# Kernel tuning notes

Hardware: AMD Instinct MI355X
Metric: run time of the kernel (lower is better)

The kernel has to match this reference:

```python
import jax, jax.numpy as jnp
import numpy as np
import math

D_MODEL = 1024
N_HEADS = 16
RANK = 16
SCALE = 16.0
T_LEN = 2048
BSZ = 2


def setup_inputs() -> dict:
    key = jax.random.key(0)
    ks = jax.random.split(key, 12)
    d, r = D_MODEL, RANK
    inp = {
        "query": jax.random.normal(ks[0], (T_LEN, BSZ, d), dtype=jnp.float32),
        "key": jax.random.normal(ks[1], (T_LEN, BSZ, d), dtype=jnp.float32),
        "value": jax.random.normal(ks[2], (T_LEN, BSZ, d), dtype=jnp.float32),
        "need_weights": 0,
        "attn_mask": 0,
        "in_proj_weight": jax.random.normal(ks[3], (3 * d, d), dtype=jnp.float32) * 0.02,
        "in_proj_bias": jax.random.normal(ks[4], (3 * d,), dtype=jnp.float32) * 0.02,
        "out_w": jax.random.normal(ks[5], (d, d), dtype=jnp.float32) * 0.02,
        "out_b": jax.random.normal(ks[6], (d,), dtype=jnp.float32) * 0.02,
        "k_a": jax.random.normal(ks[7], (r, d), dtype=jnp.float32) * 0.02,
        "k_b": jax.random.normal(ks[8], (r, d), dtype=jnp.float32) * 0.02,
        "v_a": jax.random.normal(ks[9], (r, d), dtype=jnp.float32) * 0.02,
        "v_b": jax.random.normal(ks[10], (r, d), dtype=jnp.float32) * 0.02,
    }
    return inp


def reference(query, key, value, need_weights, attn_mask,
              in_proj_weight, in_proj_bias, out_w, out_b,
              k_a, k_b, v_a, v_b):
    # NOTE: original module computes q,k,v all from `query` (self-attention);
    # `key`, `value`, `need_weights`, `attn_mask` are unused in the math.
    T, B, d = query.shape
    H = N_HEADS
    hd = d // H
    qkv = query @ in_proj_weight.T + in_proj_bias  # (T, B, 3d)
    q, k, v = jnp.split(qkv, 3, axis=-1)
    s = SCALE / RANK
    # LoRA low-rank updates on K and V (computed from query)
    k = k + s * ((query @ k_a.T) @ k_b)
    v = v + s * ((query @ v_a.T) @ v_b)
    # split heads: (T, B, H, hd)
    qh = q.reshape(T, B, H, hd)
    kh = k.reshape(T, B, H, hd)
    vh = v.reshape(T, B, H, hd)
    scale = 1.0 / math.sqrt(hd)
    scores = jnp.einsum('tbhd,sbhd->bhts', qh * scale, kh)  # (B, H, T, T)
    attn = jax.nn.softmax(scores, axis=-1)
    out = jnp.einsum('bhts,sbhd->tbhd', attn, vh).reshape(T, B, d)
    out = out @ out_w.T + out_b
    return out
```

## Files before the change

kernel.cpp:

```cpp
#include <hip/hip_runtime.h>
#include <stdint.h>

#define DEVI __device__ __forceinline__

typedef unsigned short u16;
typedef __attribute__((ext_vector_type(4))) float f32x4;
typedef __attribute__((ext_vector_type(16))) float f32x16;
typedef __attribute__((ext_vector_type(8))) short bf16x8;
typedef __attribute__((ext_vector_type(2))) unsigned int u32x2;

constexpr int T_LEN = 2048;
constexpr int BSZ   = 2;
constexpr int DM    = 1024;
constexpr int NH    = 16;
constexpr int HD    = 64;
constexpr int MROWS = T_LEN * BSZ;
constexpr float LORA_S = 16.0f / 16.0f;
constexpr float QSCALE = 0.125f * 1.4426950408889634f;

DEVI u16 f2bf(float x) {
  union { float f; uint32_t u; } v; v.f = x;
  uint32_t r = (v.u + 0x7FFFu + ((v.u >> 16) & 1u)) >> 16;
  return (u16)r;
}

DEVI uint32_t pk2bf(float a, float b) {
  return (uint32_t)f2bf(a) | ((uint32_t)f2bf(b) << 16);
}

DEVI uint32_t e2r(float x) {
  union { float f; uint32_t u; } v;
  v.f = __builtin_amdgcn_exp2f(x);
  return v.u + 0x8000u;
}

DEVI void gload_lds16(const void* g, void* l) {
  __builtin_amdgcn_global_load_lds(
      (const __attribute__((address_space(1))) void*)g,
      (__attribute__((address_space(3))) void*)l, 16, 0, 0);
}

DEVI f32x4 mfma16(bf16x8 a, bf16x8 b, f32x4 c) {
  return __builtin_amdgcn_mfma_f32_16x16x32_bf16(a, b, c, 0, 0, 0);
}
DEVI f32x16 mfma32(bf16x8 a, bf16x8 b, f32x16 c) {
  return __builtin_amdgcn_mfma_f32_32x32x16_bf16(a, b, c, 0, 0, 0);
}

DEVI int kvswz(int rc, int l) { return rc * 128 + ((l ^ (rc & 15)) << 3); }

#define WAITBAR(N)                                        \
  do {                                                    \
    asm volatile("s_waitcnt vmcnt(" #N ")" ::: "memory"); \
    __builtin_amdgcn_sched_barrier(0);                    \
    __builtin_amdgcn_s_barrier();                         \
    __builtin_amdgcn_sched_barrier(0);                    \
  } while (0)

__global__ void prep_kernel(const float* __restrict__ query,
                            const float* __restrict__ W,
                            const float* __restrict__ ka, const float* __restrict__ kb,
                            const float* __restrict__ va, const float* __restrict__ vb,
                            const float* __restrict__ ow,
                            u16* __restrict__ Wm, u16* __restrict__ Wo,
                            u16* __restrict__ Aq) {
  const int W3 = 3 * DM * DM;
  const int WO = DM * DM;
  const int AQ = MROWS * DM;
  const int total = W3 + WO + AQ;
  for (int idx = blockIdx.x * blockDim.x + threadIdx.x; idx < total;
       idx += gridDim.x * blockDim.x) {
    if (idx < W3) {
      const int n = idx >> 10, k = idx & 1023;
      float w = W[idx];
      if (n >= 2 * DM) {
        const int n2 = n - 2 * DM;
        float a = 0.f;
#pragma unroll
        for (int r = 0; r < 16; ++r) a += va[r * DM + k] * vb[r * DM + n2];
        w += LORA_S * a;
      } else if (n >= DM) {
        const int n2 = n - DM;
        float a = 0.f;
#pragma unroll
        for (int r = 0; r < 16; ++r) a += ka[r * DM + k] * kb[r * DM + n2];
        w += LORA_S * a;
      }
      Wm[idx] = f2bf(w);
    } else if (idx < W3 + WO) {
      const int i = idx - W3;
      Wo[i] = f2bf(ow[i]);
    } else {
      const int i = idx - W3 - WO;
      Aq[i] = f2bf(query[i]);
    }
  }
}

template <int EPIL>
__global__ __launch_bounds__(256) void gemm_bt(
    const u16* __restrict__ A, const u16* __restrict__ Bt,
    const float* __restrict__ bias, float* __restrict__ Cf,
    u16* __restrict__ Qb, u16* __restrict__ Kb, u16* __restrict__ Vt,
    int M, int N, int K) {
  constexpr int BM = 128, BN = 128, BK = 32;
  __shared__ alignas(16) u16 SM[4][2][4096];
  const int tid = threadIdx.x;
  const int wv = tid >> 6, ln = tid & 63;
  const int l16 = ln & 15, lhi = ln >> 4;
  const int row0 = blockIdx.x * BM, col0 = blockIdx.y * BN;
  const int wr = (wv >> 1) * 64, wc = (wv & 1) * 64;

  f32x4 acc[4][4];
#pragma unroll
  for (int i = 0; i < 4; ++i)
#pragma unroll
    for (int j = 0; j < 4; ++j) acc[i][j] = f32x4{0.f, 0.f, 0.f, 0.f};

  const int lrA = wv * 16 + (ln >> 3);
  const int lrB = lrA + 8;
  const int s_ = ln & 7;
  const int la = s_ ^ (lrA & 7), lb = s_ ^ (lrB & 7);
  const int ra = lrA + 64 * (la >> 2), ca = (la & 3) * 8;
  const int rb = lrB + 64 * (lb >> 2), cb = (lb & 3) * 8;

  const u16* pa0 = A + (size_t)(row0 + ra) * K + ca;
  const u16* pa1 = A + (size_t)(row0 + rb) * K + cb;
  const u16* pb0 = Bt + (size_t)(col0 + ra) * K + ca;
  const u16* pb1 = Bt + (size_t)(col0 + rb) * K + cb;

  auto stagep = [&](int buf) {
    gload_lds16(pa0, &SM[buf][0][(wv * 16) * 64]);
    gload_lds16(pa1, &SM[buf][0][(wv * 16 + 8) * 64]);
    gload_lds16(pb0, &SM[buf][1][(wv * 16) * 64]);
    gload_lds16(pb1, &SM[buf][1][(wv * 16 + 8) * 64]);
    pa0 += BK; pa1 += BK; pb0 += BK; pb1 += BK;
  };

  auto compute = [&](int buf) {
    const u16* Al = SM[buf][0];
    const u16* Bl = SM[buf][1];
    bf16x8 af[4], bfr[4];
#pragma unroll
    for (int m = 0; m < 4; ++m) {
      const int r = wr + m * 16 + l16, lr = r & 63;
      const int sl = (lhi | ((r >> 6) << 2)) ^ (lr & 7);
      af[m] = *(const bf16x8*)&Al[lr * 64 + sl * 8];
    }
#pragma unroll
    for (int n = 0; n < 4; ++n) {
      const int r = wc + n * 16 + l16, lr = r & 63;
      const int sl = (lhi | ((r >> 6) << 2)) ^ (lr & 7);
      bfr[n] = *(const bf16x8*)&Bl[lr * 64 + sl * 8];
    }
#pragma unroll
    for (int m = 0; m < 4; ++m)
#pragma unroll
      for (int n = 0; n < 4; ++n) acc[m][n] = mfma16(af[m], bfr[n], acc[m][n]);
  };

  const int NS = K / BK;
  stagep(0); stagep(1); stagep(2);

  for (int t4 = 0; t4 < NS - 4; t4 += 4) {
    WAITBAR(8); compute(0); stagep(3);
    WAITBAR(8); compute(1); stagep(0);
    WAITBAR(8); compute(2); stagep(1);
    WAITBAR(8); compute(3); stagep(2);
  }
  WAITBAR(8); compute(0); stagep(3);
  WAITBAR(8); compute(1);
  WAITBAR(4); compute(2);
  WAITBAR(0); compute(3);

  if constexpr (EPIL == 0) {
    if (col0 >= 2 * DM) {
      u16* Cl = (u16*)SM;
      __syncthreads();
#pragma unroll
      for (int m = 0; m < 4; ++m)
#pragma unroll
        for (int n = 0; n < 4; ++n) {
          const int lc = wc + n * 16 + l16;
          const float bc = bias[col0 + lc];
#pragma unroll
          for (int r = 0; r < 4; ++r) {
            const int rl = wr + m * 16 + lhi * 4 + r;
            const int tl = rl >> 1, bb = rl & 1;
            Cl[lc * 128 + bb * 64 + (((tl >> 3) ^ (lc & 7)) << 3) + (tl & 7)] =
                f2bf(acc[m][n][r] + bc);
          }
        }
      __syncthreads();
      const int h0 = (col0 - 2 * DM) >> 6;
      const int t0 = row0 >> 1;
#pragma unroll
      for (int i = 0; i < 8; ++i) {
        const int cid = i * 256 + tid;
        const int lc = cid >> 4, bb = (cid >> 3) & 1, tc = cid & 7;
        bf16x8 ch = *(const bf16x8*)&Cl[lc * 128 + bb * 64 + ((tc ^ (lc & 7)) << 3)];
        const int h = h0 + (lc >> 6), dd = lc & 63;
        *(bf16x8*)&Vt[(((size_t)(bb * NH + h)) * HD + dd) * T_LEN + t0 + tc * 8] = ch;
      }
      return;
    }
  }

#pragma unroll
  for (int m = 0; m < 4; ++m) {
#pragma unroll
    for (int n = 0; n < 4; ++n) {
      const int col = col0 + wc + n * 16 + l16;
      const float bc = bias[col];
#pragma unroll
      for (int r = 0; r < 4; ++r) {
        const int row = row0 + wr + m * 16 + lhi * 4 + r;
        const float v = acc[m][n][r] + bc;
        if constexpr (EPIL == 0) {
          const int t = row >> 1, b = row & 1;
          if (col < DM) {
            const int h = col >> 6, dd = col & 63;
            Qb[(((size_t)(b * NH + h)) * T_LEN + t) * HD + dd] = f2bf(v * QSCALE);
          } else {
            const int c2 = col - DM, h = c2 >> 6, dd = c2 & 63;
            Kb[(((size_t)(b * NH + h)) * T_LEN + t) * HD + dd] = f2bf(v);
          }
        } else {
          Cf[(size_t)row * N + col] = v;
        }
      }
    }
  }
}

__global__ __launch_bounds__(256) void attn_kernel(const u16* __restrict__ Qb,
                                                   const u16* __restrict__ Kb,
                                                   const u16* __restrict__ Vt,
                                                   u16* __restrict__ Ob) {
  constexpr int KBLK = 64;
  constexpr int NT = T_LEN / KBLK;
  __shared__ alignas(16) u16 KV[4][2][32 * 128];

  const int tid = threadIdx.x;
  const int wv = tid >> 6, ln = tid & 63;
  const int l32 = ln & 31, hi = ln >> 5;

  const int bid = blockIdx.x;
  const int lb = (bid & 7) * 64 + (bid >> 3);
  const int bh = lb >> 4;
  const int b = bh >> 4, h = bh & 15;
  const int q0 = (lb & 15) * 128 + wv * 32;

  const u16* Qh = Qb + (size_t)bh * T_LEN * HD;
  const u16* Kh = Kb + (size_t)bh * T_LEN * HD;
  const u16* Vh = Vt + (size_t)bh * HD * T_LEN;

  bf16x8 qf[4];
#pragma unroll
  for (int kd = 0; kd < 4; ++kd)
    qf[kd] = *(const bf16x8*)&Qh[(size_t)(q0 + l32) * HD + kd * 16 + hi * 8];

  bf16x8 ones;
#pragma unroll
  for (int i = 0; i < 8; ++i) ones[i] = (short)0x3F80;

  f32x16 ot[2] = {f32x16{}, f32x16{}};
  f32x16 lacc = f32x16{};

  const int g_row = ln >> 4;
  const int g_s   = ln & 15;
  const int j0 = wv * 2, j1 = wv * 2 + 1;
  const int row0r = 4 * j0 + g_row, row1r = 4 * j1 + g_row;
  const int l0 = g_s ^ (row0r & 15), l1 = g_s ^ (row1r & 15);
  const int lr0 = row0r + 32 * (l0 >> 3), lr1 = row1r + 32 * (l1 >> 3);
  const int c80 = (l0 & 7) * 8, c81 = (l1 & 7) * 8;

  const u16* ks0 = Kh + (size_t)lr0 * HD + c80;
  const u16* ks1 = Kh + (size_t)lr1 * HD + c81;
  const u16* vs0 = Vh + (size_t)lr0 * T_LEN + c80;
  const u16* vs1 = Vh + (size_t)lr1 * T_LEN + c81;

  auto stagep = [&](int buf) {
    gload_lds16(ks0, &KV[buf][0][j0 * 512]);
    gload_lds16(ks1, &KV[buf][0][j1 * 512]);
    gload_lds16(vs0, &KV[buf][1][j0 * 512]);
    gload_lds16(vs1, &KV[buf][1][j1 * 512]);
    ks0 += KBLK * HD; ks1 += KBLK * HD; vs0 += KBLK; vs1 += KBLK;
  };

  auto compute = [&](int buf) {
    const u16* Kl = KV[buf][0];
    const u16* Vl = KV[buf][1];
    f32x16 st[2] = {f32x16{}, f32x16{}};
#pragma unroll
    for (int kd = 0; kd < 4; ++kd) {
      bf16x8 k0 = *(const bf16x8*)&Kl[kvswz(l32, kd * 2 + hi)];
      bf16x8 k1 = *(const bf16x8*)&Kl[kvswz(l32, 8 + kd * 2 + hi)];
      st[0] = mfma32(k0, qf[kd], st[0]);
      st[1] = mfma32(k1, qf[kd], st[1]);
    }
    uint32_t c[2][8];
#pragma unroll
    for (int mk = 0; mk < 2; ++mk)
#pragma unroll
      for (int d = 0; d < 8; ++d)
        c[mk][d] = __builtin_amdgcn_perm(e2r(st[mk][2 * d + 1]),
                                         e2r(st[mk][2 * d]), 0x07060302u);
#pragma unroll
    for (int ksl = 0; ksl < 4; ++ksl) {
      const int mk = ksl >> 1, s2 = ksl & 1;
      uint32_t a0 = c[mk][4 * s2 + 0], b0 = c[mk][4 * s2 + 2];
      uint32_t a1 = c[mk][4 * s2 + 1], b1 = c[mk][4 * s2 + 3];
      u32x2 r0 = __builtin_amdgcn_permlane32_swap(a0, b0, false, false);
      u32x2 r1 = __builtin_amdgcn_permlane32_swap(a1, b1, false, false);
      union { bf16x8 v; uint32_t u[4]; } pu;
      pu.u[0] = r0[0]; pu.u[1] = r1[0]; pu.u[2] = r0[1]; pu.u[3] = r1[1];
      bf16x8 vf0 = *(const bf16x8*)&Vl[kvswz(l32, ksl * 2 + hi)];
      bf16x8 vf1 = *(const bf16x8*)&Vl[kvswz(l32, 8 + ksl * 2 + hi)];
      ot[0] = mfma32(vf0, pu.v, ot[0]);
      ot[1] = mfma32(vf1, pu.v, ot[1]);
      lacc = mfma32(ones, pu.v, lacc);
    }
  };

  stagep(0); stagep(1); stagep(2);

  for (int t4 = 0; t4 < NT - 4; t4 += 4) {
    WAITBAR(8); compute(0); stagep(3);
    WAITBAR(8); compute(1); stagep(0);
    WAITBAR(8); compute(2); stagep(1);
    WAITBAR(8); compute(3); stagep(2);
  }
  WAITBAR(8); compute(0); stagep(3);
  WAITBAR(8); compute(1);
  WAITBAR(4); compute(2);
  WAITBAR(0); compute(3);

  const float inv = 1.0f / lacc[0];
  const size_t rowbase = ((size_t)(q0 + l32) * BSZ + b) * DM + h * HD;
#pragma unroll
  for (int dt = 0; dt < 2; ++dt) {
#pragma unroll
    for (int g = 0; g < 4; ++g) {
      const float v0 = ot[dt][4 * g + 0] * inv;
      const float v1 = ot[dt][4 * g + 1] * inv;
      const float v2 = ot[dt][4 * g + 2] * inv;
      const float v3 = ot[dt][4 * g + 3] * inv;
      u32x2 w; w[0] = pk2bf(v0, v1); w[1] = pk2bf(v2, v3);
      const int dim = dt * 32 + 8 * g + 4 * hi;
      *(u32x2*)&Ob[rowbase + dim] = w;
    }
  }
}

extern "C" void kernel_launch(void* const* d_in, const int* in_sizes, int n_in,
                              void* d_out, int out_size, void* d_ws, size_t ws_size,
                              hipStream_t stream) {
  const float* query = (const float*)d_in[0];
  const float* W     = (const float*)d_in[5];
  const float* bias  = (const float*)d_in[6];
  const float* ow    = (const float*)d_in[7];
  const float* ob    = (const float*)d_in[8];
  const float* ka    = (const float*)d_in[9];
  const float* kb    = (const float*)d_in[10];
  const float* va    = (const float*)d_in[11];
  const float* vb    = (const float*)d_in[12];

  char* ws = (char*)d_ws;
  u16* Wm = (u16*)ws; ws += (size_t)3 * DM * DM * 2;
  u16* Wo = (u16*)ws; ws += (size_t)DM * DM * 2;
  u16* Aq = (u16*)ws; ws += (size_t)MROWS * DM * 2;
  u16* Qb = (u16*)ws; ws += (size_t)BSZ * NH * T_LEN * HD * 2;
  u16* Kb = (u16*)ws; ws += (size_t)BSZ * NH * T_LEN * HD * 2;
  u16* Vt = (u16*)ws; ws += (size_t)BSZ * NH * T_LEN * HD * 2;
  u16* Ob = (u16*)ws; ws += (size_t)MROWS * DM * 2;

  prep_kernel<<<2048, 256, 0, stream>>>(query, W, ka, kb, va, vb, ow, Wm, Wo, Aq);

  gemm_bt<0><<<dim3(MROWS / 128, (3 * DM) / 128), 256, 0, stream>>>(
      Aq, Wm, bias, nullptr, Qb, Kb, Vt, MROWS, 3 * DM, DM);

  attn_kernel<<<512, 256, 0, stream>>>(Qb, Kb, Vt, Ob);

  gemm_bt<1><<<dim3(MROWS / 128, DM / 128), 256, 0, stream>>>(
      Ob, Wo, ob, (float*)d_out, nullptr, nullptr, nullptr, MROWS, DM, DM);
}
```

Before: 110.4 us.

## Restructure attention KV pipeline to double-tile stages and add MFMA priority hints

The attention main loop now stages all four LDS buffers up front and processes two KV tiles per barrier pair, refilling two buffers at a time after an extra barrier. The goal is to halve the number of vmcnt-wait barriers per tile and give each wave more compute between syncs. s_setprio is raised around the MFMA sections to favour matrix issue across waves. The exp2 result is now truncated to bf16 instead of rounded, which drops one add per element at a small accuracy cost.

```diff
diff --git a/kernel.cpp b/kernel.cpp
--- a/kernel.cpp
+++ b/kernel.cpp
@@ -31,7 +31,7 @@
 DEVI uint32_t e2r(float x) {
   union { float f; uint32_t u; } v;
   v.f = __builtin_amdgcn_exp2f(x);
-  return v.u + 0x8000u;
+  return v.u;
 }
 
 DEVI void gload_lds16(const void* g, void* l) {
@@ -52,6 +52,13 @@
 #define WAITBAR(N)                                        \
   do {                                                    \
     asm volatile("s_waitcnt vmcnt(" #N ")" ::: "memory"); \
+    __builtin_amdgcn_sched_barrier(0);                    \
+    __builtin_amdgcn_s_barrier();                         \
+    __builtin_amdgcn_sched_barrier(0);                    \
+  } while (0)
+
+#define BARO()                                            \
+  do {                                                    \
     __builtin_amdgcn_sched_barrier(0);                    \
     __builtin_amdgcn_s_barrier();                         \
     __builtin_amdgcn_sched_barrier(0);                    \
@@ -115,7 +122,7 @@
 #pragma unroll
   for (int i = 0; i < 4; ++i)
 #pragma unroll
-    for (int j = 0; j < 4; ++j) acc[i][j] = f32x4{0.f, 0.f, 0.f, 0.f};
+    for (int j2 = 0; j2 < 4; ++j2) acc[i][j2] = f32x4{0.f, 0.f, 0.f, 0.f};
 
   const int lrA = wv * 16 + (ln >> 3);
   const int lrB = lrA + 8;
@@ -238,7 +245,6 @@
                                                    const u16* __restrict__ Vt,
                                                    u16* __restrict__ Ob) {
   constexpr int KBLK = 64;
-  constexpr int NT = T_LEN / KBLK;
   __shared__ alignas(16) u16 KV[4][2][32 * 128];
 
   const int tid = threadIdx.x;
@@ -292,6 +298,7 @@
     const u16* Kl = KV[buf][0];
     const u16* Vl = KV[buf][1];
     f32x16 st[2] = {f32x16{}, f32x16{}};
+    __builtin_amdgcn_s_setprio(1);
 #pragma unroll
     for (int kd = 0; kd < 4; ++kd) {
       bf16x8 k0 = *(const bf16x8*)&Kl[kvswz(l32, kd * 2 + hi)];
@@ -299,6 +306,7 @@
       st[0] = mfma32(k0, qf[kd], st[0]);
       st[1] = mfma32(k1, qf[kd], st[1]);
     }
+    __builtin_amdgcn_s_setprio(0);
     uint32_t c[2][8];
 #pragma unroll
     for (int mk = 0; mk < 2; ++mk)
@@ -306,6 +314,7 @@
       for (int d = 0; d < 8; ++d)
         c[mk][d] = __builtin_amdgcn_perm(e2r(st[mk][2 * d + 1]),
                                          e2r(st[mk][2 * d]), 0x07060302u);
+    __builtin_amdgcn_s_setprio(1);
 #pragma unroll
     for (int ksl = 0; ksl < 4; ++ksl) {
       const int mk = ksl >> 1, s2 = ksl & 1;
@@ -321,20 +330,17 @@
       ot[1] = mfma32(vf1, pu.v, ot[1]);
       lacc = mfma32(ones, pu.v, lacc);
     }
+    __builtin_amdgcn_s_setprio(0);
   };
 
-  stagep(0); stagep(1); stagep(2);
-
-  for (int t4 = 0; t4 < NT - 4; t4 += 4) {
-    WAITBAR(8); compute(0); stagep(3);
-    WAITBAR(8); compute(1); stagep(0);
-    WAITBAR(8); compute(2); stagep(1);
-    WAITBAR(8); compute(3); stagep(2);
-  }
-  WAITBAR(8); compute(0); stagep(3);
-  WAITBAR(8); compute(1);
-  WAITBAR(4); compute(2);
-  WAITBAR(0); compute(3);
+  stagep(0); stagep(1); stagep(2); stagep(3);
+
+  for (int it7 = 0; it7 < 7; ++it7) {
+    WAITBAR(8); compute(0); compute(1); BARO(); stagep(0); stagep(1);
+    WAITBAR(8); compute(2); compute(3); BARO(); stagep(2); stagep(3);
+  }
+  WAITBAR(8); compute(0); compute(1);
+  WAITBAR(0); compute(2); compute(3);
 
   const float inv = 1.0f / lacc[0];
   const size_t rowbase = ((size_t)(q0 + l32) * BSZ + b) * DM + h * HD;
```

Result: no change. 109.7 us (-0.6%).
